# Optimization experiments

Hardware: AMD Instinct MI355X
Metric: run time of the kernel (lower is better)

Reference implementation:

```python
import jax, jax.numpy as jnp
import numpy as np

HEAD_SIZE = 64
N_EMB = 384
B, S = 512, 256

def setup_inputs() -> dict:
    key = jax.random.key(0)
    k1, k2, k3, k4 = jax.random.split(key, 4)
    x = jax.random.normal(k1, (B, S, N_EMB), dtype=jnp.float32)
    scale = 1.0 / np.sqrt(N_EMB)
    Wq = jax.random.normal(k2, (N_EMB, HEAD_SIZE), dtype=jnp.float32) * scale
    Wk = jax.random.normal(k3, (N_EMB, HEAD_SIZE), dtype=jnp.float32) * scale
    Wv = jax.random.normal(k4, (N_EMB, HEAD_SIZE), dtype=jnp.float32) * scale
    return {"x": x, "Wq": Wq, "Wk": Wk, "Wv": Wv}

def reference(x, Wq, Wk, Wv):
    # Projections (Linear, no bias): [B,S,E] @ [E,H] -> [B,S,H]
    q = jnp.einsum('bse,eh->bsh', x, Wq)
    k = jnp.einsum('bse,eh->bsh', x, Wk)
    v = jnp.einsum('bse,eh->bsh', x, Wv)
    # Scores: [B,S,S], scaled by 1/sqrt(head_size)
    scores = jnp.einsum('bqh,bkh->bqk', q, k) / jnp.sqrt(jnp.asarray(HEAD_SIZE, x.dtype))
    seq_len = x.shape[1]
    causal = jnp.tril(jnp.ones((seq_len, seq_len), dtype=bool))
    scores = jnp.where(causal[None, :, :], scores, jnp.asarray(-jnp.inf, scores.dtype))
    attn = jax.nn.softmax(scores, axis=-1)
    # dropout_ratio=0 -> identity
    out = jnp.einsum('bqk,bkh->bqh', attn, v)
    return out
```

## Files before the change

### kernel.cpp

```cpp
#include <hip/hip_runtime.h>
#include <hip/hip_bf16.h>


#define NB   512
#define SS   256
#define EE   384
#define HH   64

typedef short bf16x8 __attribute__((ext_vector_type(8)));
typedef float f32x4  __attribute__((ext_vector_type(4)));

__device__ __forceinline__ short f2bf(float f) {
  union { float f; unsigned u; } x; x.f = f;
  unsigned r = x.u + 0x7fffu + ((x.u >> 16) & 1u);
  return (short)(r >> 16);
}

__global__ __launch_bounds__(256) void prep_w_kernel(
    const float* __restrict__ Wq, const float* __restrict__ Wk,
    const float* __restrict__ Wv, short* __restrict__ wfrag) {
  int t = blockIdx.x * 256 + threadIdx.x;
  if (t >= 12 * 12 * 64) return;
  int ks  = t / (12 * 64);
  int rem = t % (12 * 64);
  int nf  = rem / 64;
  int l   = rem % 64;
  int l15 = l & 15, lhi = l >> 4;
  int ncat = nf * 16 + l15;
  const float* W = (ncat < 64) ? Wq : (ncat < 128 ? Wk : Wv);
  int n = ncat & 63;
  short* dst = wfrag + (size_t)t * 8;
#pragma unroll
  for (int j = 0; j < 8; ++j) {
    int kk = ks * 32 + lhi * 8 + j;
    dst[j] = f2bf(W[kk * 64 + n]);
  }
}

__global__ __launch_bounds__(384, 3) void fused_kernel(
    const float* __restrict__ x, const short* __restrict__ wfrag,
    short* __restrict__ qws, float* __restrict__ out) {
  __shared__ __align__(16) short Kl[SS * HH];
  __shared__ __align__(16) short Vt[HH * SS];
  __shared__ __align__(16) short xst[16 * EE];

  int b    = blockIdx.x;
  int tid  = threadIdx.x;
  int lane = tid & 63, wv = tid >> 6;
  int l15  = lane & 15, lhi = lane >> 4;
  int sw   = l15 & 7;
  const float* xb = x + (size_t)b * SS * EE;
  short* qbb = qws + (size_t)b * SS * HH;

  bf16x8 af[12][2];
#pragma unroll
  for (int ks = 0; ks < 12; ++ks)
#pragma unroll
    for (int ht = 0; ht < 2; ++ht)
      af[ks][ht] = *(const bf16x8*)(wfrag + ((size_t)(ks * 12 + wv * 2 + ht) * 64 + lane) * 8);

  f32x4 st[4];
  auto loadch = [&](int ch) {
    const float* p0 = xb + (size_t)ch * 16 * EE;
#pragma unroll
    for (int i = 0; i < 4; ++i)
      st[i] = *(const f32x4*)(p0 + (size_t)(tid + 384 * i) * 4);
  };
  auto writech = [&]() {
#pragma unroll
    for (int i = 0; i < 4; ++i) {
      int c16 = tid + 384 * i;
      int row = c16 / 96, cg4 = c16 % 96;
      union { short4 s4; __hip_bfloat162 h2[2]; } u;
      u.h2[0] = __float22bfloat162_rn(make_float2(st[i][0], st[i][1]));
      u.h2[1] = __float22bfloat162_rn(make_float2(st[i][2], st[i][3]));
      *(short4*)(xst + row * 384 + (((cg4 >> 1) ^ (row & 7)) * 8 + (cg4 & 1) * 4)) = u.s4;
    }
  };

  loadch(0);
  writech();
  for (int ch = 0; ch < 16; ++ch) {
    __syncthreads();
    if (ch < 15) loadch(ch + 1);

    f32x4 acc[2];
    acc[0] = (f32x4){0.f, 0.f, 0.f, 0.f};
    acc[1] = (f32x4){0.f, 0.f, 0.f, 0.f};
#pragma unroll
    for (int ks = 0; ks < 12; ++ks) {
      bf16x8 bx = *(const bf16x8*)(xst + l15 * 384 + (((ks * 4 + lhi) ^ sw) * 8));
      acc[0] = __builtin_amdgcn_mfma_f32_16x16x32_bf16(af[ks][0], bx, acc[0], 0, 0, 0);
      acc[1] = __builtin_amdgcn_mfma_f32_16x16x32_bf16(af[ks][1], bx, acc[1], 0, 0, 0);
    }

    int row  = ch * 16 + l15;
    int srow = ((row & 8) >> 1) | (row & 3);
#pragma unroll
    for (int ht = 0; ht < 2; ++ht) {
      int f = wv * 2 + ht;
      int ncat = f * 16 + lhi * 4;
      if (f < 4) {
        union { short4 s4; __hip_bfloat162 h2[2]; } oq;
        oq.h2[0] = __float22bfloat162_rn(make_float2(acc[ht][0], acc[ht][1]));
        oq.h2[1] = __float22bfloat162_rn(make_float2(acc[ht][2], acc[ht][3]));
        *(short4*)(qbb + (size_t)row * HH + ncat) = oq.s4;
      } else if (f < 8) {
        int col = ncat - 64;
        union { short4 s4; __hip_bfloat162 h2[2]; } ok;
        ok.h2[0] = __float22bfloat162_rn(make_float2(acc[ht][0], acc[ht][1]));
        ok.h2[1] = __float22bfloat162_rn(make_float2(acc[ht][2], acc[ht][3]));
        *(short4*)(Kl + row * 64 + (col ^ (srow << 3))) = ok.s4;
      } else {
#pragma unroll
        for (int j = 0; j < 4; ++j) {
          int h = ncat - 128 + j;
          Vt[h * 256 + (row ^ ((h & 7) << 3))] = f2bf(acc[ht][j]);
        }
      }
    }
    __syncthreads();
    if (ch < 15) writech();
  }
  __syncthreads();

  size_t obase = (size_t)b * SS * HH;
#pragma unroll
  for (int u = 0; u < 3; ++u) {
    if (u == 2 && wv >= 4) continue;
    int rt;
    if (u == 0)      rt = (wv < 4) ? (13 - wv) : (19 - wv);
    else if (u == 1) rt = (wv < 2) ? (5 - wv) : ((wv < 4) ? (6 + wv) : (2 + wv));
    else             rt = (wv < 2) ? (2 + wv) : (wv - 2);

    int qrow0 = rt * 16;
    int twp   = (rt + 2) & ~1;
    int nk    = twp >> 1;
    int qg    = qrow0 + l15;

    const short* qrow = qbb + (size_t)(qrow0 + l15) * HH;
    bf16x8 qa0 = *(const bf16x8*)(qrow + lhi * 8);
    bf16x8 qa1 = *(const bf16x8*)(qrow + 32 + lhi * 8);

    f32x4 s[16];
#pragma unroll
    for (int t = 0; t < 16; ++t) {
      if (t >= twp) continue;
      int kc = (t >> 1) * 32 + ((l15 >> 2) << 3) + ((t & 1) << 2) + (l15 & 3);
      const short* kp = Kl + kc * 64;
      bf16x8 kb0 = *(const bf16x8*)(kp + ((lhi * 8) ^ (sw << 3)));
      bf16x8 kb1 = *(const bf16x8*)(kp + ((32 + lhi * 8) ^ (sw << 3)));
      f32x4 a = (f32x4){0.f, 0.f, 0.f, 0.f};
      a = __builtin_amdgcn_mfma_f32_16x16x32_bf16(kb0, qa0, a, 0, 0, 0);
      a = __builtin_amdgcn_mfma_f32_16x16x32_bf16(kb1, qa1, a, 0, 0, 0);
#pragma unroll
      for (int r = 0; r < 4; ++r) {
        int kg = (t >> 1) * 32 + lhi * 8 + ((t & 1) << 2) + r;
        s[t][r] = (kg <= qg) ? a[r] * 0.125f : -INFINITY;
      }
    }

    float mx = -3.0e38f;
#pragma unroll
    for (int t = 0; t < 16; ++t) {
      if (t >= twp) continue;
#pragma unroll
      for (int r = 0; r < 4; ++r) mx = fmaxf(mx, s[t][r]);
    }
    mx = fmaxf(mx, __shfl_xor(mx, 16));
    mx = fmaxf(mx, __shfl_xor(mx, 32));
    float sm = 0.f;
#pragma unroll
    for (int t = 0; t < 16; ++t) {
      if (t >= twp) continue;
#pragma unroll
      for (int r = 0; r < 4; ++r) {
        float p = __expf(s[t][r] - mx);
        s[t][r] = p;
        sm += p;
      }
    }
    sm += __shfl_xor(sm, 16);
    sm += __shfl_xor(sm, 32);
    float inv = 1.f / sm;
    float invq[4];
#pragma unroll
    for (int r = 0; r < 4; ++r) invq[r] = __shfl(inv, lhi * 4 + r);

    f32x4 o[4];
#pragma unroll
    for (int nf = 0; nf < 4; ++nf) o[nf] = (f32x4){0.f, 0.f, 0.f, 0.f};
#pragma unroll
    for (int kc2 = 0; kc2 < 8; ++kc2) {
      if (kc2 >= nk) continue;
      union { bf16x8 v; __hip_bfloat162 h2[4]; } pu;
      pu.h2[0] = __float22bfloat162_rn(make_float2(s[2*kc2][0],   s[2*kc2][1]));
      pu.h2[1] = __float22bfloat162_rn(make_float2(s[2*kc2][2],   s[2*kc2][3]));
      pu.h2[2] = __float22bfloat162_rn(make_float2(s[2*kc2+1][0], s[2*kc2+1][1]));
      pu.h2[3] = __float22bfloat162_rn(make_float2(s[2*kc2+1][2], s[2*kc2+1][3]));
      int kofs = kc2 * 32 + lhi * 8;
#pragma unroll
      for (int nf = 0; nf < 4; ++nf) {
        int hrow = nf * 16 + l15;
        bf16x8 vb = *(const bf16x8*)(Vt + hrow * 256 + (kofs ^ ((hrow & 7) << 3)));
        o[nf] = __builtin_amdgcn_mfma_f32_16x16x32_bf16(pu.v, vb, o[nf], 0, 0, 0);
      }
    }

#pragma unroll
    for (int nf = 0; nf < 4; ++nf)
#pragma unroll
      for (int r = 0; r < 4; ++r) {
        int q = qrow0 + lhi * 4 + r;
        int h = nf * 16 + l15;
        out[obase + (size_t)q * HH + h] = o[nf][r] * invq[r];
      }
  }
}

extern "C" void kernel_launch(void* const* d_in, const int* in_sizes, int n_in,
                              void* d_out, int out_size, void* d_ws, size_t ws_size,
                              hipStream_t stream) {
  const float* x  = (const float*)d_in[0];
  const float* Wq = (const float*)d_in[1];
  const float* Wk = (const float*)d_in[2];
  const float* Wv = (const float*)d_in[3];
  float* out = (float*)d_out;

  char* ws = (char*)d_ws;
  short* wfrag = (short*)ws;
  short* qws   = (short*)(ws + 262144);

  prep_w_kernel<<<36, 256, 0, stream>>>(Wq, Wk, Wv, wfrag);
  fused_kernel<<<512, 384, 0, stream>>>(x, wfrag, qws, out);
}
```

Before: 68.10 us.

## Load x directly to registers, keep Q in LDS, use 512-thread blocks

Replaces the shared-memory staging of x chunks, which needed two block barriers per chunk, with direct per-wave register loads and conversion into MFMA operands. Work is split into two groups of four waves, each covering half the sequence rows and three output fragments. Q now stays in a swizzled LDS buffer instead of a global workspace round trip. The attention phase uses 8 waves with paired row tiles for causal balance. The block grows to 512 threads with more registers per thread and 96KB of LDS, which may reduce occupancy, and the x reads are now strided per lane rather than fully coalesced.

New measurement: 114.7 us. 1.68x slower.

```diff
diff --git a/kernel.cpp b/kernel.cpp
--- a/kernel.cpp
+++ b/kernel.cpp
@@ -37,74 +37,73 @@
   }
 }
 
-__global__ __launch_bounds__(384, 3) void fused_kernel(
+__global__ __launch_bounds__(512, 2) void fused_kernel(
     const float* __restrict__ x, const short* __restrict__ wfrag,
-    short* __restrict__ qws, float* __restrict__ out) {
+    float* __restrict__ out) {
+  __shared__ __align__(16) short Ql[SS * HH];
   __shared__ __align__(16) short Kl[SS * HH];
   __shared__ __align__(16) short Vt[HH * SS];
-  __shared__ __align__(16) short xst[16 * EE];
 
   int b    = blockIdx.x;
   int tid  = threadIdx.x;
   int lane = tid & 63, wv = tid >> 6;
   int l15  = lane & 15, lhi = lane >> 4;
   int sw   = l15 & 7;
+  int g    = wv >> 2;
+  int wg   = wv & 3;
   const float* xb = x + (size_t)b * SS * EE;
-  short* qbb = qws + (size_t)b * SS * HH;
-
-  bf16x8 af[12][2];
+
+  bf16x8 af[12][3];
 #pragma unroll
   for (int ks = 0; ks < 12; ++ks)
 #pragma unroll
-    for (int ht = 0; ht < 2; ++ht)
-      af[ks][ht] = *(const bf16x8*)(wfrag + ((size_t)(ks * 12 + wv * 2 + ht) * 64 + lane) * 8);
-
-  f32x4 st[4];
-  auto loadch = [&](int ch) {
-    const float* p0 = xb + (size_t)ch * 16 * EE;
-#pragma unroll
-    for (int i = 0; i < 4; ++i)
-      st[i] = *(const f32x4*)(p0 + (size_t)(tid + 384 * i) * 4);
-  };
-  auto writech = [&]() {
-#pragma unroll
-    for (int i = 0; i < 4; ++i) {
-      int c16 = tid + 384 * i;
-      int row = c16 / 96, cg4 = c16 % 96;
-      union { short4 s4; __hip_bfloat162 h2[2]; } u;
-      u.h2[0] = __float22bfloat162_rn(make_float2(st[i][0], st[i][1]));
-      u.h2[1] = __float22bfloat162_rn(make_float2(st[i][2], st[i][3]));
-      *(short4*)(xst + row * 384 + (((cg4 >> 1) ^ (row & 7)) * 8 + (cg4 & 1) * 4)) = u.s4;
-    }
-  };
-
-  loadch(0);
-  writech();
-  for (int ch = 0; ch < 16; ++ch) {
-    __syncthreads();
-    if (ch < 15) loadch(ch + 1);
-
-    f32x4 acc[2];
-    acc[0] = (f32x4){0.f, 0.f, 0.f, 0.f};
-    acc[1] = (f32x4){0.f, 0.f, 0.f, 0.f};
+    for (int ht = 0; ht < 3; ++ht)
+      af[ks][ht] = *(const bf16x8*)(wfrag + ((size_t)(ks * 12 + wg * 3 + ht) * 64 + lane) * 8);
+
+  const float* prow = xb + (size_t)(g * 128 + l15) * EE + lhi * 8;
+
+  for (int rt = 0; rt < 8; ++rt) {
+    const float* pr = prow + (size_t)rt * 16 * EE;
+
+    f32x4 pf[6][2];
+#pragma unroll
+    for (int i = 0; i < 6; ++i) {
+      pf[i][0] = *(const f32x4*)(pr + i * 32);
+      pf[i][1] = *(const f32x4*)(pr + i * 32 + 4);
+    }
+
+    f32x4 acc[3];
+#pragma unroll
+    for (int ht = 0; ht < 3; ++ht) acc[ht] = (f32x4){0.f, 0.f, 0.f, 0.f};
+
 #pragma unroll
     for (int ks = 0; ks < 12; ++ks) {
-      bf16x8 bx = *(const bf16x8*)(xst + l15 * 384 + (((ks * 4 + lhi) ^ sw) * 8));
-      acc[0] = __builtin_amdgcn_mfma_f32_16x16x32_bf16(af[ks][0], bx, acc[0], 0, 0, 0);
-      acc[1] = __builtin_amdgcn_mfma_f32_16x16x32_bf16(af[ks][1], bx, acc[1], 0, 0, 0);
-    }
-
-    int row  = ch * 16 + l15;
+      int slot = ks % 6;
+      union { bf16x8 v; __hip_bfloat162 h2[4]; } u;
+      u.h2[0] = __float22bfloat162_rn(make_float2(pf[slot][0][0], pf[slot][0][1]));
+      u.h2[1] = __float22bfloat162_rn(make_float2(pf[slot][0][2], pf[slot][0][3]));
+      u.h2[2] = __float22bfloat162_rn(make_float2(pf[slot][1][0], pf[slot][1][1]));
+      u.h2[3] = __float22bfloat162_rn(make_float2(pf[slot][1][2], pf[slot][1][3]));
+      if (ks < 6) {
+        pf[slot][0] = *(const f32x4*)(pr + (ks + 6) * 32);
+        pf[slot][1] = *(const f32x4*)(pr + (ks + 6) * 32 + 4);
+      }
+#pragma unroll
+      for (int ht = 0; ht < 3; ++ht)
+        acc[ht] = __builtin_amdgcn_mfma_f32_16x16x32_bf16(af[ks][ht], u.v, acc[ht], 0, 0, 0);
+    }
+
+    int row  = g * 128 + rt * 16 + l15;
     int srow = ((row & 8) >> 1) | (row & 3);
 #pragma unroll
-    for (int ht = 0; ht < 2; ++ht) {
-      int f = wv * 2 + ht;
+    for (int ht = 0; ht < 3; ++ht) {
+      int f = wg * 3 + ht;
       int ncat = f * 16 + lhi * 4;
       if (f < 4) {
         union { short4 s4; __hip_bfloat162 h2[2]; } oq;
         oq.h2[0] = __float22bfloat162_rn(make_float2(acc[ht][0], acc[ht][1]));
         oq.h2[1] = __float22bfloat162_rn(make_float2(acc[ht][2], acc[ht][3]));
-        *(short4*)(qbb + (size_t)row * HH + ncat) = oq.s4;
+        *(short4*)(Ql + row * 64 + (ncat ^ ((row & 7) << 3))) = oq.s4;
       } else if (f < 8) {
         int col = ncat - 64;
         union { short4 s4; __hip_bfloat162 h2[2]; } ok;
@@ -119,28 +118,21 @@
         }
       }
     }
-    __syncthreads();
-    if (ch < 15) writech();
   }
   __syncthreads();
 
   size_t obase = (size_t)b * SS * HH;
 #pragma unroll
-  for (int u = 0; u < 3; ++u) {
-    if (u == 2 && wv >= 4) continue;
-    int rt;
-    if (u == 0)      rt = (wv < 4) ? (13 - wv) : (19 - wv);
-    else if (u == 1) rt = (wv < 2) ? (5 - wv) : ((wv < 4) ? (6 + wv) : (2 + wv));
-    else             rt = (wv < 2) ? (2 + wv) : (wv - 2);
-
+  for (int u = 0; u < 2; ++u) {
+    int rt    = (u == 0) ? wv : (15 - wv);
     int qrow0 = rt * 16;
     int twp   = (rt + 2) & ~1;
     int nk    = twp >> 1;
     int qg    = qrow0 + l15;
 
-    const short* qrow = qbb + (size_t)(qrow0 + l15) * HH;
-    bf16x8 qa0 = *(const bf16x8*)(qrow + lhi * 8);
-    bf16x8 qa1 = *(const bf16x8*)(qrow + 32 + lhi * 8);
+    int qlrow = qrow0 + l15;
+    bf16x8 qa0 = *(const bf16x8*)(Ql + qlrow * 64 + ((lhi * 8) ^ ((qlrow & 7) << 3)));
+    bf16x8 qa1 = *(const bf16x8*)(Ql + qlrow * 64 + ((32 + lhi * 8) ^ ((qlrow & 7) << 3)));
 
     f32x4 s[16];
 #pragma unroll
@@ -227,10 +219,8 @@
   const float* Wv = (const float*)d_in[3];
   float* out = (float*)d_out;
 
-  char* ws = (char*)d_ws;
-  short* wfrag = (short*)ws;
-  short* qws   = (short*)(ws + 262144);
+  short* wfrag = (short*)d_ws;
 
   prep_w_kernel<<<36, 256, 0, stream>>>(Wq, Wk, Wv, wfrag);
-  fused_kernel<<<512, 384, 0, stream>>>(x, wfrag, qws, out);
-}
+  fused_kernel<<<512, 512, 0, stream>>>(x, wfrag, out);
+}
```

## Keep Q in LDS and split projection across two wave groups per block

Applied to the files above, without the earlier changes.

Doubles the block to 768 threads. Two groups of six waves each project half of the sequence, using their own double-buffered x staging tiles. Q is now kept in a swizzled LDS buffer instead of going out to a global workspace and back. The causal attention row tiles are reassigned so ten waves handle one or two tiles each. This removes the global round trip for Q and adds overlap in staging, but it raises LDS use to about 144KB, leaving one block per CU. The launch bound of (768, 3) may also force tight register limits and spills.

Result: slower. 79.18 us (+16.3%).

```diff
diff --git a/kernel.cpp b/kernel.cpp
--- a/kernel.cpp
+++ b/kernel.cpp
@@ -37,74 +37,78 @@
   }
 }
 
-__global__ __launch_bounds__(384, 3) void fused_kernel(
+__global__ __launch_bounds__(768, 3) void fused_kernel(
     const float* __restrict__ x, const short* __restrict__ wfrag,
-    short* __restrict__ qws, float* __restrict__ out) {
+    float* __restrict__ out) {
+  __shared__ __align__(16) short Ql[SS * HH];
   __shared__ __align__(16) short Kl[SS * HH];
   __shared__ __align__(16) short Vt[HH * SS];
-  __shared__ __align__(16) short xst[16 * EE];
+  __shared__ __align__(16) short xst[4 * 16 * EE];
 
   int b    = blockIdx.x;
   int tid  = threadIdx.x;
   int lane = tid & 63, wv = tid >> 6;
   int l15  = lane & 15, lhi = lane >> 4;
   int sw   = l15 & 7;
+  int g    = wv / 6;
+  int wg   = wv % 6;
+  int tg   = tid - g * 384;
   const float* xb = x + (size_t)b * SS * EE;
-  short* qbb = qws + (size_t)b * SS * HH;
 
   bf16x8 af[12][2];
 #pragma unroll
   for (int ks = 0; ks < 12; ++ks)
 #pragma unroll
     for (int ht = 0; ht < 2; ++ht)
-      af[ks][ht] = *(const bf16x8*)(wfrag + ((size_t)(ks * 12 + wv * 2 + ht) * 64 + lane) * 8);
+      af[ks][ht] = *(const bf16x8*)(wfrag + ((size_t)(ks * 12 + wg * 2 + ht) * 64 + lane) * 8);
 
   f32x4 st[4];
   auto loadch = [&](int ch) {
-    const float* p0 = xb + (size_t)ch * 16 * EE;
+    const float* p0 = xb + (size_t)(g * 128 + ch * 16) * EE;
 #pragma unroll
     for (int i = 0; i < 4; ++i)
-      st[i] = *(const f32x4*)(p0 + (size_t)(tid + 384 * i) * 4);
+      st[i] = *(const f32x4*)(p0 + (size_t)(tg + 384 * i) * 4);
   };
-  auto writech = [&]() {
+  auto writech = [&](short* xl) {
 #pragma unroll
     for (int i = 0; i < 4; ++i) {
-      int c16 = tid + 384 * i;
+      int c16 = tg + 384 * i;
       int row = c16 / 96, cg4 = c16 % 96;
       union { short4 s4; __hip_bfloat162 h2[2]; } u;
       u.h2[0] = __float22bfloat162_rn(make_float2(st[i][0], st[i][1]));
       u.h2[1] = __float22bfloat162_rn(make_float2(st[i][2], st[i][3]));
-      *(short4*)(xst + row * 384 + (((cg4 >> 1) ^ (row & 7)) * 8 + (cg4 & 1) * 4)) = u.s4;
+      *(short4*)(xl + row * 384 + (((cg4 >> 1) ^ (row & 7)) * 8 + (cg4 & 1) * 4)) = u.s4;
     }
   };
 
   loadch(0);
-  writech();
-  for (int ch = 0; ch < 16; ++ch) {
+  writech(xst + (g * 2) * (16 * EE));
+  for (int ch = 0; ch < 8; ++ch) {
     __syncthreads();
-    if (ch < 15) loadch(ch + 1);
+    if (ch < 7) loadch(ch + 1);
+    const short* xl = xst + (g * 2 + (ch & 1)) * (16 * EE);
 
     f32x4 acc[2];
     acc[0] = (f32x4){0.f, 0.f, 0.f, 0.f};
     acc[1] = (f32x4){0.f, 0.f, 0.f, 0.f};
 #pragma unroll
     for (int ks = 0; ks < 12; ++ks) {
-      bf16x8 bx = *(const bf16x8*)(xst + l15 * 384 + (((ks * 4 + lhi) ^ sw) * 8));
+      bf16x8 bx = *(const bf16x8*)(xl + l15 * 384 + (((ks * 4 + lhi) ^ sw) * 8));
       acc[0] = __builtin_amdgcn_mfma_f32_16x16x32_bf16(af[ks][0], bx, acc[0], 0, 0, 0);
       acc[1] = __builtin_amdgcn_mfma_f32_16x16x32_bf16(af[ks][1], bx, acc[1], 0, 0, 0);
     }
 
-    int row  = ch * 16 + l15;
+    int row  = g * 128 + ch * 16 + l15;
     int srow = ((row & 8) >> 1) | (row & 3);
 #pragma unroll
     for (int ht = 0; ht < 2; ++ht) {
-      int f = wv * 2 + ht;
+      int f = wg * 2 + ht;
       int ncat = f * 16 + lhi * 4;
       if (f < 4) {
         union { short4 s4; __hip_bfloat162 h2[2]; } oq;
         oq.h2[0] = __float22bfloat162_rn(make_float2(acc[ht][0], acc[ht][1]));
         oq.h2[1] = __float22bfloat162_rn(make_float2(acc[ht][2], acc[ht][3]));
-        *(short4*)(qbb + (size_t)row * HH + ncat) = oq.s4;
+        *(short4*)(Ql + row * 64 + (ncat ^ ((row & 7) << 3))) = oq.s4;
       } else if (f < 8) {
         int col = ncat - 64;
         union { short4 s4; __hip_bfloat162 h2[2]; } ok;
@@ -120,27 +124,26 @@
       }
     }
     __syncthreads();
-    if (ch < 15) writech();
+    if (ch < 7) writech(xst + (g * 2 + ((ch + 1) & 1)) * (16 * EE));
   }
   __syncthreads();
 
+  int nt, rt0 = 0, rt1 = 0;
+  if (wv < 4)       { nt = 1; rt0 = 15 - wv; }
+  else if (wv < 10) { nt = 2; rt0 = 15 - wv; rt1 = wv - 4; }
+  else              { nt = 0; }
+
   size_t obase = (size_t)b * SS * HH;
-#pragma unroll
-  for (int u = 0; u < 3; ++u) {
-    if (u == 2 && wv >= 4) continue;
-    int rt;
-    if (u == 0)      rt = (wv < 4) ? (13 - wv) : (19 - wv);
-    else if (u == 1) rt = (wv < 2) ? (5 - wv) : ((wv < 4) ? (6 + wv) : (2 + wv));
-    else             rt = (wv < 2) ? (2 + wv) : (wv - 2);
-
+  for (int u = 0; u < nt; ++u) {
+    int rt    = (u == 0) ? rt0 : rt1;
     int qrow0 = rt * 16;
     int twp   = (rt + 2) & ~1;
     int nk    = twp >> 1;
     int qg    = qrow0 + l15;
 
-    const short* qrow = qbb + (size_t)(qrow0 + l15) * HH;
-    bf16x8 qa0 = *(const bf16x8*)(qrow + lhi * 8);
-    bf16x8 qa1 = *(const bf16x8*)(qrow + 32 + lhi * 8);
+    int qlrow = qrow0 + l15;
+    bf16x8 qa0 = *(const bf16x8*)(Ql + qlrow * 64 + ((lhi * 8) ^ ((qlrow & 7) << 3)));
+    bf16x8 qa1 = *(const bf16x8*)(Ql + qlrow * 64 + ((32 + lhi * 8) ^ ((qlrow & 7) << 3)));
 
     f32x4 s[16];
 #pragma unroll
@@ -227,10 +230,8 @@
   const float* Wv = (const float*)d_in[3];
   float* out = (float*)d_out;
 
-  char* ws = (char*)d_ws;
-  short* wfrag = (short*)ws;
-  short* qws   = (short*)(ws + 262144);
+  short* wfrag = (short*)d_ws;
 
   prep_w_kernel<<<36, 256, 0, stream>>>(Wq, Wk, Wv, wfrag);
-  fused_kernel<<<512, 384, 0, stream>>>(x, wfrag, qws, out);
-}
+  fused_kernel<<<512, 768, 0, stream>>>(x, wfrag, out);
+}
```
